# Kernel optimization log

Hardware: AMD Instinct MI355X
Metric: run time of the kernel (lower is better)

The kernel has to match this reference:

```python
import jax, jax.numpy as jnp
import numpy as np

N, L, D_IN = 8192, 32, 256   # total paths, max path len, token+method embed
E, H, T, C = 128, 128, 128, 2  # encode_size, hidden_dim, test_vector_size, label_count
G = 1024                      # number of methods (groups)
LN_EPS = 1e-5


def _lstm_last_hidden(xs, lengths, Wih, Whh, bih, bhh):
    """Single-layer LSTM over padded [N,L,E]; returns h at t=length-1 per row (packed-sequence h_n)."""
    xs_t = jnp.transpose(xs, (1, 0, 2))  # [L, N, E]
    n = xs.shape[0]
    h0 = jnp.zeros((n, H), xs.dtype)
    c0 = jnp.zeros((n, H), xs.dtype)

    def step(carry, inp):
        h, c = carry
        x_t, t = inp
        gates = x_t @ Wih.T + bih + h @ Whh.T + bhh  # [N, 4H], torch gate order i,f,g,o
        i, f, g, o = jnp.split(gates, 4, axis=-1)
        c_new = jax.nn.sigmoid(f) * c + jax.nn.sigmoid(i) * jnp.tanh(g)
        h_new = jax.nn.sigmoid(o) * jnp.tanh(c_new)
        valid = (t < lengths)[:, None]  # freeze state past each path's length
        return (jnp.where(valid, h_new, h), jnp.where(valid, c_new, c)), None

    (h_last, _), _ = jax.lax.scan(step, (h0, c0), (xs_t, jnp.arange(L)))
    return h_last  # [N, H]


def setup_inputs() -> dict:
    key = jax.random.key(0)
    ks = jax.random.split(key, 10)
    rng = np.random.default_rng(0)

    inputs = jax.random.normal(ks[0], (N, L, D_IN), dtype=jnp.float32)
    path_lengths = jnp.asarray(rng.integers(1, L + 1, size=N), dtype=jnp.int32)
    # sorted segment ids, every group non-empty (torch.split groups are contiguous and >=1)
    ids = np.sort(np.concatenate([np.arange(G), rng.integers(0, G, size=N - G)]))
    segment_ids = jnp.asarray(ids, dtype=jnp.int32)

    s = 0.05
    W_in = jax.random.normal(ks[1], (E, D_IN), dtype=jnp.float32) * s
    ln_gamma = jnp.ones((E,), jnp.float32)
    ln_beta = jnp.zeros((E,), jnp.float32)
    Wih = jax.random.normal(ks[2], (4 * H, E), dtype=jnp.float32) * s
    Whh = jax.random.normal(ks[3], (4 * H, H), dtype=jnp.float32) * s
    bih = jax.random.normal(ks[4], (4 * H,), dtype=jnp.float32) * s
    bhh = jax.random.normal(ks[5], (4 * H,), dtype=jnp.float32) * s
    attn_param = jax.random.normal(ks[6], (H,), dtype=jnp.float32) * s
    W_out = jax.random.normal(ks[7], (T, H), dtype=jnp.float32) * s
    W_cls = jax.random.normal(ks[8], (C, T), dtype=jnp.float32) * s

    return {"inputs": inputs, "path_lengths": path_lengths, "segment_ids": segment_ids,
            "W_in": W_in, "ln_gamma": ln_gamma, "ln_beta": ln_beta,
            "Wih": Wih, "Whh": Whh, "bih": bih, "bhh": bhh,
            "attn_param": attn_param, "W_out": W_out, "W_cls": W_cls}


def reference(inputs, path_lengths, segment_ids, W_in, ln_gamma, ln_beta,
              Wih, Whh, bih, bhh, attn_param, W_out, W_cls):
    # input projection + layernorm + tanh (dropout disabled, p=0)
    x = inputs @ W_in.T  # [N, L, E]
    mu = jnp.mean(x, axis=-1, keepdims=True)
    var = jnp.mean((x - mu) ** 2, axis=-1, keepdims=True)
    x = jnp.tanh((x - mu) * jax.lax.rsqrt(var + LN_EPS) * ln_gamma + ln_beta)

    h = _lstm_last_hidden(x, path_lengths, Wih, Whh, bih, bhh)  # [N, H]

    # segmented softmax attention + mean over each group's paths
    logits = h @ attn_param  # [N]
    m = jax.ops.segment_max(logits, segment_ids, num_segments=G)
    e = jnp.exp(logits - m[segment_ids])
    Z = jax.ops.segment_sum(e, segment_ids, num_segments=G)
    attn = e / Z[segment_ids]  # per-group softmax weights
    wsum = jax.ops.segment_sum(attn[:, None] * h, segment_ids, num_segments=G)  # [G, H]
    counts = jax.ops.segment_sum(jnp.ones_like(logits), segment_ids, num_segments=G)
    code = wsum / counts[:, None]  # torch.mean divides by group size

    code_vectors = code @ W_out.T  # [G, T]
    outputs = code_vectors @ W_cls.T  # [G, C]
    return outputs, code_vectors, attn_param
```

## Files before the change

### kernel.cpp

```cpp
#include <hip/hip_runtime.h>


#define NPATH 8192
#define LMAX  32
#define DIN   256
#define EDIM  128
#define HDIM  128
#define NGRP  1024
#define NTOK  (NPATH * LMAX)
#define NCHUNK 512
#define XSLAB ((long)NPATH * EDIM)

typedef __attribute__((ext_vector_type(8))) short short8;
typedef __attribute__((ext_vector_type(4))) short s16x4;
typedef __attribute__((ext_vector_type(4))) float f32x4;

__device__ __forceinline__ unsigned short f2bf(float f) {
    unsigned int x = __float_as_uint(f);
    x += 0x7fffu + ((x >> 16) & 1u);
    return (unsigned short)(x >> 16);
}
__device__ __forceinline__ float sigmoid_f(float x) {
    return __fdividef(1.f, 1.f + __expf(-x));
}
__device__ __forceinline__ float tanh_f(float x) {
    float t = __expf(-2.f * x);
    return __fdividef(2.f, 1.f + t) - 1.f;
}

__global__ __launch_bounds__(512) void k0_sort(const int* __restrict__ lens,
                                               int* __restrict__ perm,
                                               int* __restrict__ inv) {
    __shared__ int hw[8][LMAX];
    __shared__ int startg[8][LMAX];
    __shared__ int colsum[LMAX];
    __shared__ int binoff[LMAX];
    const int tid = threadIdx.x;
    const int w = tid >> 6, lane = tid & 63;
    if (lane < LMAX) hw[w][lane] = 0;
    __syncthreads();
    for (int i = tid; i < NPATH; i += 512)
        atomicAdd(&hw[w][lens[i] - 1], 1);
    __syncthreads();
    if (tid < LMAX) {
        int s = 0;
        #pragma unroll
        for (int ww = 0; ww < 8; ++ww) { startg[ww][tid] = s; s += hw[ww][tid]; }
        colsum[tid] = s;
    }
    __syncthreads();
    if (tid == 0) {
        int s = 0;
        for (int b = 0; b < LMAX; ++b) { binoff[b] = s; s += colsum[b]; }
    }
    __syncthreads();
    if (tid < LMAX) {
        #pragma unroll
        for (int ww = 0; ww < 8; ++ww) startg[ww][tid] += binoff[tid];
    }
    __syncthreads();
    for (int i = tid; i < NPATH; i += 512) {
        int b = lens[i] - 1;
        int p = atomicAdd(&startg[w][b], 1);
        perm[p] = i;
        inv[i] = p;
    }
}

#define K1_ROWS 128
#define K1_PAD  264
__global__ __launch_bounds__(512) void k1_proj(
    const float* __restrict__ inp, const float* __restrict__ Win,
    const float* __restrict__ gam, const float* __restrict__ bet,
    const int* __restrict__ inv, unsigned short* __restrict__ xt)
{
    __shared__ short As[K1_ROWS * K1_PAD];
    __shared__ short Bs[EDIM * K1_PAD];
    const int tid = threadIdx.x;
    const long m0 = (long)blockIdx.x * K1_ROWS;

    #pragma unroll
    for (int i = 0; i < 16; ++i) {
        int chunk = i * 512 + tid;
        int row = chunk >> 6, c4 = chunk & 63;
        float4 v = *(const float4*)&Win[row * DIN + c4 * 4];
        s16x4 s = { (short)f2bf(v.x), (short)f2bf(v.y), (short)f2bf(v.z), (short)f2bf(v.w) };
        *(s16x4*)&Bs[row * K1_PAD + c4 * 4] = s;
    }
    #pragma unroll
    for (int i = 0; i < 16; ++i) {
        int chunk = i * 512 + tid;
        int row = chunk >> 6, c4 = chunk & 63;
        float4 v = *(const float4*)&inp[(m0 + row) * DIN + c4 * 4];
        s16x4 s = { (short)f2bf(v.x), (short)f2bf(v.y), (short)f2bf(v.z), (short)f2bf(v.w) };
        *(s16x4*)&As[row * K1_PAD + c4 * 4] = s;
    }
    __syncthreads();

    const int w = tid >> 6, lane = tid & 63, q = lane >> 4, c = lane & 15;
    const f32x4 fzero = {0.f, 0.f, 0.f, 0.f};
    f32x4 acc[8];
    #pragma unroll
    for (int nt = 0; nt < 8; ++nt) acc[nt] = fzero;

    const short* arow = &As[(w * 16 + c) * K1_PAD + q * 8];
    const short* brow = &Bs[c * K1_PAD + q * 8];
    #pragma unroll
    for (int ks = 0; ks < 8; ++ks) {
        short8 a = *(const short8*)(arow + ks * 32);
        #pragma unroll
        for (int nt = 0; nt < 8; ++nt) {
            short8 b = *(const short8*)(brow + nt * 16 * K1_PAD + ks * 32);
            acc[nt] = __builtin_amdgcn_mfma_f32_16x16x32_bf16(a, b, acc[nt], 0, 0, 0);
        }
    }

    float gr[8], br[8];
    #pragma unroll
    for (int nt = 0; nt < 8; ++nt) { int col = nt * 16 + c; gr[nt] = gam[col]; br[nt] = bet[col]; }
    const int tok0 = w * 16 + q * 4;
    const int slot = inv[(int)((m0 + tok0) >> 5)];
    const int tbase = tok0 & 31;
    #pragma unroll
    for (int r = 0; r < 4; ++r) {
        float s = 0.f, ss = 0.f;
        #pragma unroll
        for (int nt = 0; nt < 8; ++nt) { float v = acc[nt][r]; s += v; ss += v * v; }
        #pragma unroll
        for (int m = 1; m < 16; m <<= 1) { s += __shfl_xor(s, m, 64); ss += __shfl_xor(ss, m, 64); }
        float mu = s * (1.f / 128.f);
        float var = ss * (1.f / 128.f) - mu * mu;
        float rstd = rsqrtf(var + 1e-5f);
        unsigned short* orow = &xt[(long)(tbase + r) * XSLAB + (long)slot * EDIM];
        #pragma unroll
        for (int nt = 0; nt < 8; ++nt) {
            float v = (acc[nt][r] - mu) * rstd * gr[nt] + br[nt];
            orow[nt * 16 + c] = f2bf(tanh_f(v));
        }
    }
}

__global__ __launch_bounds__(512, 2) void k2_lstm(
    const unsigned short* __restrict__ xt,
    const float* __restrict__ Wih, const float* __restrict__ Whh,
    const float* __restrict__ bih, const float* __restrict__ bhh,
    const int* __restrict__ lens, const int* __restrict__ perm,
    float* __restrict__ h_last)
{
    __shared__ unsigned short wih_s[512 * 128];
    __shared__ unsigned short hb[2][16 * 128];
    __shared__ unsigned short xb[2][16 * 128];
    __shared__ int pemb[16];
    __shared__ int lenb[16];
    const int tid = threadIdx.x;
    const int w = tid >> 6, lane = tid & 63, q = lane >> 4, c = lane & 15;
    const int xr = (c & 7) << 3;

    #pragma unroll
    for (int i = 0; i < 32; ++i) {
        int chunk = i * 512 + tid;
        int j = chunk >> 5, c4 = chunk & 31;
        float4 v = *(const float4*)&Wih[j * EDIM + c4 * 4];
        s16x4 s = { (short)f2bf(v.x), (short)f2bf(v.y), (short)f2bf(v.z), (short)f2bf(v.w) };
        *(s16x4*)&wih_s[j * 128 + ((c4 * 4) ^ ((j & 7) << 3))] = s;
    }

    short8 whf[4][4];
    float bs[4];
    #pragma unroll
    for (int g = 0; g < 4; ++g) {
        const int j = g * 128 + w * 16 + c;
        bs[g] = bih[j] + bhh[j];
        const float* ph = Whh + (long)j * HDIM + q * 8;
        #pragma unroll
        for (int ks = 0; ks < 4; ++ks) {
            float4 b0 = *(const float4*)(ph + ks * 32);
            float4 b1 = *(const float4*)(ph + ks * 32 + 4);
            short8 u;
            u[0] = (short)f2bf(b0.x); u[1] = (short)f2bf(b0.y);
            u[2] = (short)f2bf(b0.z); u[3] = (short)f2bf(b0.w);
            u[4] = (short)f2bf(b1.x); u[5] = (short)f2bf(b1.y);
            u[6] = (short)f2bf(b1.z); u[7] = (short)f2bf(b1.w);
            whf[g][ks] = u;
        }
    }

    int koff[4];
    #pragma unroll
    for (int ks = 0; ks < 4; ++ks) koff[ks] = (q * 8 + ks * 32) ^ xr;
    const unsigned short* wbase[4];
    #pragma unroll
    for (int g = 0; g < 4; ++g) wbase[g] = &wih_s[(g * 128 + w * 16 + c) * 128];

    const int srow = tid >> 5;
    const int scol = (tid * 4) & 127;
    const int sdst = srow * 128 + (scol ^ ((srow & 7) << 3));

    for (int half = 0; half < 2; ++half) {
        const int cid = half ? (NCHUNK - 1 - (int)blockIdx.x) : (int)blockIdx.x;
        const int r0 = cid * 16;
        if (tid < 16) { int p = perm[r0 + tid]; pemb[tid] = p; lenb[tid] = lens[p]; }
        { s16x4 z = {0, 0, 0, 0}; *(s16x4*)&hb[0][tid * 4] = z; }
        {
            s16x4 v = *(const s16x4*)&xt[(long)r0 * EDIM + tid * 4];
            *(s16x4*)&xb[0][sdst] = v;
        }
        __syncthreads();

        int steps = 1;
        #pragma unroll
        for (int i = 0; i < 16; ++i) steps = (lenb[i] > steps) ? lenb[i] : steps;
        int lenr[4];
        #pragma unroll
        for (int r = 0; r < 4; ++r) lenr[r] = lenb[q * 4 + r];

        float c_reg[4] = {0.f, 0.f, 0.f, 0.f};
        float h_reg[4] = {0.f, 0.f, 0.f, 0.f};

        int cur = 0;
        for (int t = 0; t < steps; ++t) {
            const int tn = (t + 1 < steps) ? (t + 1) : t;
            s16x4 xg = *(const s16x4*)&xt[(long)tn * XSLAB + (long)r0 * EDIM + tid * 4];

            f32x4 acc[4];
            #pragma unroll
            for (int g = 0; g < 4; ++g) {
                f32x4 a = {bs[g], bs[g], bs[g], bs[g]};
                acc[g] = a;
            }
            if (t) {
                short8 ha[4];
                #pragma unroll
                for (int ks = 0; ks < 4; ++ks)
                    ha[ks] = *(const short8*)&hb[cur][c * 128 + koff[ks]];
                #pragma unroll
                for (int ks = 0; ks < 4; ++ks)
                    #pragma unroll
                    for (int g = 0; g < 4; ++g)
                        acc[g] = __builtin_amdgcn_mfma_f32_16x16x32_bf16(ha[ks], whf[g][ks], acc[g], 0, 0, 0);
            }
            #pragma unroll
            for (int ks = 0; ks < 4; ++ks) {
                short8 xa = *(const short8*)&xb[cur][c * 128 + koff[ks]];
                #pragma unroll
                for (int g = 0; g < 4; ++g) {
                    short8 b = *(const short8*)(wbase[g] + koff[ks]);
                    acc[g] = __builtin_amdgcn_mfma_f32_16x16x32_bf16(xa, b, acc[g], 0, 0, 0);
                }
            }
            const int nxt = cur ^ 1;
            *(s16x4*)&xb[nxt][sdst] = xg;

            #pragma unroll
            for (int r = 0; r < 4; ++r) {
                float cn = sigmoid_f(acc[1][r]) * c_reg[r]
                         + sigmoid_f(acc[0][r]) * tanh_f(acc[2][r]);
                float hn = sigmoid_f(acc[3][r]) * tanh_f(cn);
                if (t < lenr[r]) { c_reg[r] = cn; h_reg[r] = hn; }
                const int row = q * 4 + r;
                hb[nxt][row * 128 + ((w * 16 + c) ^ ((row & 7) << 3))] = f2bf(h_reg[r]);
            }
            __syncthreads();
            cur = nxt;
        }
        #pragma unroll
        for (int r = 0; r < 4; ++r)
            h_last[(long)pemb[q * 4 + r] * HDIM + w * 16 + c] = h_reg[r];
        if (half == 0) __syncthreads();
    }
}

__global__ __launch_bounds__(64) void k3_attn(
    const float* __restrict__ h_last, const int* __restrict__ seg,
    const float* __restrict__ attn, const float* __restrict__ Wout,
    const float* __restrict__ Wcls, float* __restrict__ out)
{
    __shared__ float code_s[128];
    const int g = blockIdx.x, l = threadIdx.x;

    int lo, hi;
    { int a = 0, b = NPATH; while (a < b) { int m = (a + b) >> 1; if (seg[m] < g) a = m + 1; else b = m; } lo = a; }
    { int a = lo, b = NPATH; while (a < b) { int m = (a + b) >> 1; if (seg[m] < g + 1) a = m + 1; else b = m; } hi = a; }

    float a0 = attn[l], a1 = attn[l + 64];
    float mrun = -1e30f, Z = 0.f;
    for (int n = lo; n < hi; ++n) {
        const float* hr = &h_last[(long)n * HDIM];
        float v = hr[l] * a0 + hr[l + 64] * a1;
        #pragma unroll
        for (int m = 1; m < 64; m <<= 1) v += __shfl_xor(v, m, 64);
        float nm = fmaxf(mrun, v);
        Z = Z * __expf(mrun - nm) + __expf(v - nm);
        mrun = nm;
    }
    float w0 = 0.f, w1 = 0.f;
    for (int n = lo; n < hi; ++n) {
        const float* hr = &h_last[(long)n * HDIM];
        float v = hr[l] * a0 + hr[l + 64] * a1;
        #pragma unroll
        for (int m = 1; m < 64; m <<= 1) v += __shfl_xor(v, m, 64);
        float at = __expf(v - mrun) / Z;
        w0 += at * hr[l]; w1 += at * hr[l + 64];
    }
    float inv_cnt = (hi > lo) ? 1.f / (float)(hi - lo) : 0.f;
    code_s[l] = w0 * inv_cnt; code_s[l + 64] = w1 * inv_cnt;
    __syncthreads();

    float cv0 = 0.f, cv1 = 0.f;
    for (int k = 0; k < 128; ++k) {
        float ck = code_s[k];
        cv0 += ck * Wout[l * 128 + k];
        cv1 += ck * Wout[(l + 64) * 128 + k];
    }
    out[2048 + g * 128 + l]      = cv0;
    out[2048 + g * 128 + l + 64] = cv1;

    float p0 = cv0 * Wcls[l] + cv1 * Wcls[l + 64];
    float p1 = cv0 * Wcls[128 + l] + cv1 * Wcls[128 + l + 64];
    #pragma unroll
    for (int m = 1; m < 64; m <<= 1) { p0 += __shfl_xor(p0, m, 64); p1 += __shfl_xor(p1, m, 64); }
    if (l == 0) { out[g * 2 + 0] = p0; out[g * 2 + 1] = p1; }
    if (g == 0) { out[133120 + l] = attn[l]; out[133120 + 64 + l] = attn[l + 64]; }
}

extern "C" void kernel_launch(void* const* d_in, const int* in_sizes, int n_in,
                              void* d_out, int out_size, void* d_ws, size_t ws_size,
                              hipStream_t stream) {
    const float* inp  = (const float*)d_in[0];
    const int*   lens = (const int*)d_in[1];
    const int*   seg  = (const int*)d_in[2];
    const float* Win  = (const float*)d_in[3];
    const float* gam  = (const float*)d_in[4];
    const float* bet  = (const float*)d_in[5];
    const float* Wih  = (const float*)d_in[6];
    const float* Whh  = (const float*)d_in[7];
    const float* bih  = (const float*)d_in[8];
    const float* bhh  = (const float*)d_in[9];
    const float* attn = (const float*)d_in[10];
    const float* Wout = (const float*)d_in[11];
    const float* Wcls = (const float*)d_in[12];

    unsigned short* xt = (unsigned short*)d_ws;
    float* h_last = (float*)((char*)d_ws + (size_t)NTOK * EDIM * 2);
    int* perm = (int*)((char*)d_ws + (size_t)NTOK * EDIM * 2
                                   + (size_t)NPATH * HDIM * 4);
    int* inv  = perm + NPATH;

    hipLaunchKernelGGL(k0_sort, dim3(1), dim3(512), 0, stream, lens, perm, inv);
    hipLaunchKernelGGL(k1_proj, dim3(NTOK / K1_ROWS), dim3(512), 0, stream, inp, Win, gam, bet, inv, xt);
    hipLaunchKernelGGL(k2_lstm, dim3(NCHUNK / 2), dim3(512), 0, stream,
                       xt, Wih, Whh, bih, bhh, lens, perm, h_last);
    hipLaunchKernelGGL(k3_attn, dim3(NGRP), dim3(64), 0, stream, h_last, seg, attn, Wout, Wcls,
                       (float*)d_out);
}
```

Measured before the change: 537.2 us.

## Make projection kernel persistent with double-buffered input tiles and swizzled LDS

The input projection kernel now runs 256 persistent blocks. Each block loads the bf16 W_in tile into LDS once and then loops over 16 row tiles of 64 tokens. The next tile's global loads are issued before the current tile's MFMA work and stored into a second LDS buffer. LDS uses an XOR swizzle instead of padding, the layernorm reduction is split across two waves through a small LDS exchange, and results are staged in LDS so xt is written with 16-byte vector stores instead of scattered 2-byte stores. This removes the per-block weight reload and the uncoalesced output writes. In exchange it adds extra barriers and LDS traffic, and the fixed grid of 256 blocks may limit parallelism.

```diff
diff --git a/kernel.cpp b/kernel.cpp
--- a/kernel.cpp
+++ b/kernel.cpp
@@ -10,6 +10,8 @@
 #define NTOK  (NPATH * LMAX)
 #define NCHUNK 512
 #define XSLAB ((long)NPATH * EDIM)
+#define K1_TILE 64
+#define K1_TPB  16
 
 typedef __attribute__((ext_vector_type(8))) short short8;
 typedef __attribute__((ext_vector_type(4))) short s16x4;
@@ -67,75 +69,144 @@
     }
 }
 
-#define K1_ROWS 128
-#define K1_PAD  264
-__global__ __launch_bounds__(512) void k1_proj(
+__global__ __launch_bounds__(512, 2) void k1_proj(
     const float* __restrict__ inp, const float* __restrict__ Win,
     const float* __restrict__ gam, const float* __restrict__ bet,
     const int* __restrict__ inv, unsigned short* __restrict__ xt)
 {
-    __shared__ short As[K1_ROWS * K1_PAD];
-    __shared__ short Bs[EDIM * K1_PAD];
+    __shared__ unsigned short Bs[EDIM * DIN];
+    __shared__ unsigned short As[2][K1_TILE * DIN];
+    __shared__ float lnx[2][K1_TILE][2];
     const int tid = threadIdx.x;
-    const long m0 = (long)blockIdx.x * K1_ROWS;
-
-    #pragma unroll
-    for (int i = 0; i < 16; ++i) {
-        int chunk = i * 512 + tid;
-        int row = chunk >> 6, c4 = chunk & 63;
-        float4 v = *(const float4*)&Win[row * DIN + c4 * 4];
-        s16x4 s = { (short)f2bf(v.x), (short)f2bf(v.y), (short)f2bf(v.z), (short)f2bf(v.w) };
-        *(s16x4*)&Bs[row * K1_PAD + c4 * 4] = s;
-    }
-    #pragma unroll
-    for (int i = 0; i < 16; ++i) {
-        int chunk = i * 512 + tid;
-        int row = chunk >> 6, c4 = chunk & 63;
-        float4 v = *(const float4*)&inp[(m0 + row) * DIN + c4 * 4];
-        s16x4 s = { (short)f2bf(v.x), (short)f2bf(v.y), (short)f2bf(v.z), (short)f2bf(v.w) };
-        *(s16x4*)&As[row * K1_PAD + c4 * 4] = s;
-    }
-    __syncthreads();
-
     const int w = tid >> 6, lane = tid & 63, q = lane >> 4, c = lane & 15;
-    const f32x4 fzero = {0.f, 0.f, 0.f, 0.f};
-    f32x4 acc[8];
-    #pragma unroll
-    for (int nt = 0; nt < 8; ++nt) acc[nt] = fzero;
-
-    const short* arow = &As[(w * 16 + c) * K1_PAD + q * 8];
-    const short* brow = &Bs[c * K1_PAD + q * 8];
-    #pragma unroll
-    for (int ks = 0; ks < 8; ++ks) {
-        short8 a = *(const short8*)(arow + ks * 32);
-        #pragma unroll
-        for (int nt = 0; nt < 8; ++nt) {
-            short8 b = *(const short8*)(brow + nt * 16 * K1_PAD + ks * 32);
-            acc[nt] = __builtin_amdgcn_mfma_f32_16x16x32_bf16(a, b, acc[nt], 0, 0, 0);
-        }
-    }
-
-    float gr[8], br[8];
-    #pragma unroll
-    for (int nt = 0; nt < 8; ++nt) { int col = nt * 16 + c; gr[nt] = gam[col]; br[nt] = bet[col]; }
-    const int tok0 = w * 16 + q * 4;
-    const int slot = inv[(int)((m0 + tok0) >> 5)];
-    const int tbase = tok0 & 31;
-    #pragma unroll
-    for (int r = 0; r < 4; ++r) {
-        float s = 0.f, ss = 0.f;
-        #pragma unroll
-        for (int nt = 0; nt < 8; ++nt) { float v = acc[nt][r]; s += v; ss += v * v; }
-        #pragma unroll
-        for (int m = 1; m < 16; m <<= 1) { s += __shfl_xor(s, m, 64); ss += __shfl_xor(ss, m, 64); }
-        float mu = s * (1.f / 128.f);
-        float var = ss * (1.f / 128.f) - mu * mu;
-        float rstd = rsqrtf(var + 1e-5f);
-        unsigned short* orow = &xt[(long)(tbase + r) * XSLAB + (long)slot * EDIM];
-        #pragma unroll
-        for (int nt = 0; nt < 8; ++nt) {
-            float v = (acc[nt][r] - mu) * rstd * gr[nt] + br[nt];
-            orow[nt * 16 + c] = f2bf(tanh_f(v));
+    const int rg = w >> 1, ch = w & 1;
+    const int xr = (c & 7) << 3;
+
+    {
+        const int row = tid >> 2, c0 = (tid & 3) * 64;
+        const float* src = Win + row * DIN + c0;
+        const int key = (row & 7) << 3;
+        #pragma unroll
+        for (int j = 0; j < 8; ++j) {
+            float4 u0 = *(const float4*)(src + j * 8);
+            float4 u1 = *(const float4*)(src + j * 8 + 4);
+            short8 s;
+            s[0] = (short)f2bf(u0.x); s[1] = (short)f2bf(u0.y);
+            s[2] = (short)f2bf(u0.z); s[3] = (short)f2bf(u0.w);
+            s[4] = (short)f2bf(u1.x); s[5] = (short)f2bf(u1.y);
+            s[6] = (short)f2bf(u1.z); s[7] = (short)f2bf(u1.w);
+            *(short8*)&Bs[row * DIN + ((c0 + j * 8) ^ key)] = s;
+        }
+    }
+
+    const int arow = tid >> 3, ac0 = (tid & 7) * 32;
+    const int akey = (arow & 7) << 3;
+    const long tile0 = (long)blockIdx.x * K1_TPB;
+
+    float gr[4], br[4];
+    #pragma unroll
+    for (int i = 0; i < 4; ++i) {
+        int col = ch * 64 + i * 16 + c;
+        gr[i] = gam[col]; br[i] = bet[col];
+    }
+
+    {
+        const float* src = inp + (tile0 * K1_TILE + arow) * DIN + ac0;
+        #pragma unroll
+        for (int j = 0; j < 4; ++j) {
+            float4 u0 = *(const float4*)(src + j * 8);
+            float4 u1 = *(const float4*)(src + j * 8 + 4);
+            short8 s;
+            s[0] = (short)f2bf(u0.x); s[1] = (short)f2bf(u0.y);
+            s[2] = (short)f2bf(u0.z); s[3] = (short)f2bf(u0.w);
+            s[4] = (short)f2bf(u1.x); s[5] = (short)f2bf(u1.y);
+            s[6] = (short)f2bf(u1.z); s[7] = (short)f2bf(u1.w);
+            *(short8*)&As[0][arow * DIN + ((ac0 + j * 8) ^ akey)] = s;
+        }
+    }
+    __syncthreads();
+
+    for (int it = 0; it < K1_TPB; ++it) {
+        const int cur = it & 1, nxt = cur ^ 1;
+        unsigned short* Acur = &As[0][0] + cur * (K1_TILE * DIN);
+        unsigned short* Anxt = &As[0][0] + nxt * (K1_TILE * DIN);
+
+        float4 fr[8];
+        if (it + 1 < K1_TPB) {
+            const float* src = inp + ((tile0 + it + 1) * K1_TILE + arow) * DIN + ac0;
+            #pragma unroll
+            for (int j = 0; j < 8; ++j) fr[j] = *(const float4*)(src + j * 4);
+        }
+
+        f32x4 acc[4];
+        const f32x4 fzero = {0.f, 0.f, 0.f, 0.f};
+        #pragma unroll
+        for (int i = 0; i < 4; ++i) acc[i] = fzero;
+        const unsigned short* arow_p = &Acur[(rg * 16 + c) * DIN];
+        #pragma unroll
+        for (int ks = 0; ks < 8; ++ks) {
+            short8 a = *(const short8*)(arow_p + ((q * 8 + ks * 32) ^ xr));
+            #pragma unroll
+            for (int i = 0; i < 4; ++i) {
+                short8 b = *(const short8*)&Bs[(ch * 64 + i * 16 + c) * DIN
+                                               + ((q * 8 + ks * 32) ^ xr)];
+                acc[i] = __builtin_amdgcn_mfma_f32_16x16x32_bf16(a, b, acc[i], 0, 0, 0);
+            }
+        }
+
+        float sr[4], qr[4];
+        #pragma unroll
+        for (int r = 0; r < 4; ++r) {
+            float s = 0.f, ss = 0.f;
+            #pragma unroll
+            for (int i = 0; i < 4; ++i) { float v = acc[i][r]; s += v; ss += v * v; }
+            #pragma unroll
+            for (int m = 1; m < 16; m <<= 1) { s += __shfl_xor(s, m, 64); ss += __shfl_xor(ss, m, 64); }
+            sr[r] = s; qr[r] = ss;
+            if (c == 0) { lnx[ch][rg * 16 + q * 4 + r][0] = s; lnx[ch][rg * 16 + q * 4 + r][1] = ss; }
+        }
+        __syncthreads();
+
+        #pragma unroll
+        for (int r = 0; r < 4; ++r) {
+            const int grow = rg * 16 + q * 4 + r;
+            float s = sr[r] + lnx[ch ^ 1][grow][0];
+            float ss = qr[r] + lnx[ch ^ 1][grow][1];
+            float mu = s * (1.f / 128.f);
+            float rstd = rsqrtf(ss * (1.f / 128.f) - mu * mu + 1e-5f);
+            const int key = (grow & 7) << 3;
+            #pragma unroll
+            for (int i = 0; i < 4; ++i) {
+                float v = (acc[i][r] - mu) * rstd * gr[i] + br[i];
+                Acur[grow * DIN + ((ch * 64 + i * 16 + c) ^ key)] = f2bf(tanh_f(v));
+            }
+        }
+
+        if (it + 1 < K1_TPB) {
+            #pragma unroll
+            for (int j = 0; j < 4; ++j) {
+                float4 u0 = fr[j * 2], u1 = fr[j * 2 + 1];
+                short8 s;
+                s[0] = (short)f2bf(u0.x); s[1] = (short)f2bf(u0.y);
+                s[2] = (short)f2bf(u0.z); s[3] = (short)f2bf(u0.w);
+                s[4] = (short)f2bf(u1.x); s[5] = (short)f2bf(u1.y);
+                s[6] = (short)f2bf(u1.z); s[7] = (short)f2bf(u1.w);
+                *(short8*)&Anxt[arow * DIN + ((ac0 + j * 8) ^ akey)] = s;
+            }
+        }
+        __syncthreads();
+
+        {
+            const int row = tid >> 3, e0 = (tid & 7) * 16;
+            const int key = (row & 7) << 3;
+            short8 v0 = *(const short8*)&Acur[row * DIN + (e0 ^ key)];
+            short8 v1 = *(const short8*)&Acur[row * DIN + ((e0 + 8) ^ key)];
+            const long m = (tile0 + it) * K1_TILE + row;
+            const int path = (int)(m >> 5), t = (int)(m & 31);
+            const int slot = inv[path];
+            unsigned short* dst = &xt[(long)t * XSLAB + (long)slot * EDIM + e0];
+            *(short8*)dst = v0;
+            *(short8*)(dst + 8) = v1;
         }
     }
 }
@@ -347,7 +418,7 @@
     int* inv  = perm + NPATH;
 
     hipLaunchKernelGGL(k0_sort, dim3(1), dim3(512), 0, stream, lens, perm, inv);
-    hipLaunchKernelGGL(k1_proj, dim3(NTOK / K1_ROWS), dim3(512), 0, stream, inp, Win, gam, bet, inv, xt);
+    hipLaunchKernelGGL(k1_proj, dim3(256), dim3(512), 0, stream, inp, Win, gam, bet, inv, xt);
     hipLaunchKernelGGL(k2_lstm, dim3(NCHUNK / 2), dim3(512), 0, stream,
                        xt, Wih, Whh, bih, bhh, lens, perm, h_last);
     hipLaunchKernelGGL(k3_attn, dim3(NGRP), dim3(64), 0, stream, h_last, seg, attn, Wout, Wcls,
```

Result: no change. 541.4 us (+0.8%).
